# Optimization experiments

Measured on AMD Instinct MI355X. Metric: run time of the kernel, lower is better.

Reference implementation:

```python
import jax, jax.numpy as jnp
import numpy as np
import math

N_HEADS = 4
N_KV_GROUPS = 1
HEAD_DIM = 256
SLIDING_WINDOW = 512
ROPE_BASE = 1000000.0
EPS = 1e-6


def _rmsnorm(x, gamma):
    # normalize over last dim (head_dim), torch nn.RMSNorm semantics
    ms = jnp.mean(jnp.square(x), axis=-1, keepdims=True)
    return x * jax.lax.rsqrt(ms + EPS) * gamma


def _rope_tables(T, head_dim, dtype):
    inv_freq = 1.0 / (ROPE_BASE ** (jnp.arange(0, head_dim, 2, dtype=jnp.float32) / head_dim))
    t = jnp.arange(T, dtype=jnp.float32)
    freqs = jnp.outer(t, inv_freq)          # [T, head_dim/2]
    return jnp.cos(freqs).astype(dtype), jnp.sin(freqs).astype(dtype)


def _apply_rope(x, cos, sin):
    # x: [B, T, H, hd]; cos/sin: [T, hd/2] broadcast as [1, T, 1, hd/2]
    x0 = x[..., 0::2]
    x1 = x[..., 1::2]
    c = cos[None, :, None, :]
    s = sin[None, :, None, :]
    even = x0 * c - x1 * s
    odd = x0 * s + x1 * c
    return jnp.stack((even, odd), axis=-1).reshape(x.shape)


def setup_inputs() -> dict:
    key = jax.random.key(0)
    ks = jax.random.split(key, 5)
    B, T, C = 2, 4096, 1024
    scale = 0.02
    return {
        "x": jax.random.normal(ks[0], (B, T, C), dtype=jnp.float32),
        "Wq": jax.random.normal(ks[1], (C, C), dtype=jnp.float32) * scale,
        "Wk": jax.random.normal(ks[2], (N_KV_GROUPS * HEAD_DIM, C), dtype=jnp.float32) * scale,
        "Wv": jax.random.normal(ks[3], (N_KV_GROUPS * HEAD_DIM, C), dtype=jnp.float32) * scale,
        "Wo": jax.random.normal(ks[4], (C, C), dtype=jnp.float32) * scale,
        "q_gamma": jnp.ones((HEAD_DIM,), dtype=jnp.float32),
        "k_gamma": jnp.ones((HEAD_DIM,), dtype=jnp.float32),
    }


def reference(x, Wq, Wk, Wv, Wo, q_gamma, k_gamma):
    B, T, C = x.shape
    H, G, hd = N_HEADS, N_KV_GROUPS, HEAD_DIM
    rep = H // G

    q = (x @ Wq.T).reshape(B, T, H, hd)
    k = (x @ Wk.T).reshape(B, T, G, hd)
    v = (x @ Wv.T).reshape(B, T, G, hd)

    q = _rmsnorm(q, q_gamma)
    k = _rmsnorm(k, k_gamma)

    cos, sin = _rope_tables(T, hd, q.dtype)
    q = _apply_rope(q, cos, sin)
    k = _apply_rope(k, cos, sin)

    q = q.transpose(0, 2, 1, 3)                 # [B, H, T, hd]
    k = k.transpose(0, 2, 1, 3)                 # [B, G, T, hd]
    v = v.transpose(0, 2, 1, 3)
    k = jnp.repeat(k, rep, axis=1)              # [B, H, T, hd]
    v = jnp.repeat(v, rep, axis=1)

    scores = jnp.einsum("bhqd,bhkd->bhqk", q, k) / math.sqrt(hd)
    i = jnp.arange(T)[:, None]
    j = jnp.arange(T)[None, :]
    allowed = (j <= i) & (j >= i - SLIDING_WINDOW)   # causal sliding window
    scores = jnp.where(allowed, scores, -jnp.inf)
    attn = jax.nn.softmax(scores, axis=-1)
    out = jnp.einsum("bhqk,bhkd->bhqd", attn, v)     # [B, H, T, hd]
    out = out.transpose(0, 2, 1, 3).reshape(B, T, C)
    return out @ Wo.T
```

## Files before the change

### kernel.cpp

```cpp
#include <hip/hip_runtime.h>
#include <cstdint>
#include <cstddef>

#define T_SEQ 4096
#define NB    2
#define CDIM  1024
#define HD    256
#define NH    4

typedef __attribute__((ext_vector_type(8))) __bf16 bf16x8;
typedef __attribute__((ext_vector_type(4))) __bf16 bf16x4;
typedef __attribute__((ext_vector_type(4))) float  floatx4;

__device__ __forceinline__ floatx4 mfma16(bf16x8 a, bf16x8 b, floatx4 c) {
  return __builtin_amdgcn_mfma_f32_16x16x32_bf16(a, b, c, 0, 0, 0);
}

__device__ __forceinline__ void gl2lds16(const void* g, void* l) {
  __builtin_amdgcn_global_load_lds(
      (__attribute__((address_space(1))) void*)g,
      (__attribute__((address_space(3))) void*)l, 16, 0, 0);
}

__global__ __launch_bounds__(256) void cvt_all(const float* __restrict__ x,
                                               const float* __restrict__ wq,
                                               const float* __restrict__ wk,
                                               const float* __restrict__ wv,
                                               const float* __restrict__ wo,
                                               __bf16* __restrict__ xb,
                                               __bf16* __restrict__ wb,
                                               __bf16* __restrict__ wob) {
  int i = blockIdx.x * 256 + threadIdx.x;
  const float* src;
  __bf16* dst;
  int off;
  if (i < 2097152)      { src = x;  dst = xb;            off = i; }
  else if (i < 2359296) { src = wq; dst = wb;            off = i - 2097152; }
  else if (i < 2424832) { src = wk; dst = wb + 1048576;  off = i - 2359296; }
  else if (i < 2490368) { src = wv; dst = wb + 1310720;  off = i - 2424832; }
  else                  { src = wo; dst = wob;           off = i - 2490368; }
  float4 v = ((const float4*)src)[off];
  bf16x4 o;
  o[0] = (__bf16)v.x; o[1] = (__bf16)v.y; o[2] = (__bf16)v.z; o[3] = (__bf16)v.w;
  *(bf16x4*)&dst[(size_t)off * 4] = o;
}

template <typename OutT>
__global__ __launch_bounds__(256) void gemm_bt(const __bf16* __restrict__ A,
                                               const __bf16* __restrict__ B,
                                               OutT* __restrict__ C,
                                               int M, int N, int K) {
  __shared__ __bf16 As[128 * 64];
  __shared__ __bf16 Bs[128 * 64];
  const int tid  = threadIdx.x;
  const int lane = tid & 63;
  const int wave = tid >> 6;
  const int wm = wave >> 1, wn = wave & 1;
  const int lrow = lane & 15, quad = lane >> 4;
  const int bm = blockIdx.y, bn = blockIdx.x;

  const __bf16* gA = A + (size_t)(bm * 128) * K;
  const __bf16* gB = B + (size_t)(bn * 128) * K;
  const int arow = tid >> 3;
  const int acol = ((tid & 7) ^ ((tid >> 3) & 7)) * 8;
  const int l7 = lrow & 7;

  floatx4 acc[4][4] = {};

  for (int kt = 0; kt < K; kt += 64) {
#pragma unroll
    for (int i = 0; i < 4; ++i)
      gl2lds16(gA + (size_t)(i * 32 + arow) * K + kt + acol, &As[i * 2048 + tid * 8]);
#pragma unroll
    for (int i = 0; i < 4; ++i)
      gl2lds16(gB + (size_t)(i * 32 + arow) * K + kt + acol, &Bs[i * 2048 + tid * 8]);
    __syncthreads();
#pragma unroll
    for (int kk = 0; kk < 2; ++kk) {
      bf16x8 af[4], bfr[4];
#pragma unroll
      for (int mi = 0; mi < 4; ++mi)
        af[mi] = *(const bf16x8*)&As[(wm * 64 + mi * 16 + lrow) * 64 +
                                     ((kk * 4 + quad) ^ l7) * 8];
#pragma unroll
      for (int ni = 0; ni < 4; ++ni)
        bfr[ni] = *(const bf16x8*)&Bs[(wn * 64 + ni * 16 + lrow) * 64 +
                                      ((kk * 4 + quad) ^ l7) * 8];
#pragma unroll
      for (int mi = 0; mi < 4; ++mi)
#pragma unroll
        for (int ni = 0; ni < 4; ++ni)
          acc[mi][ni] = mfma16(af[mi], bfr[ni], acc[mi][ni]);
    }
    __syncthreads();
  }

  const int row0 = bm * 128 + wm * 64;
  const int col0 = bn * 128 + wn * 64;
#pragma unroll
  for (int mi = 0; mi < 4; ++mi)
#pragma unroll
    for (int ni = 0; ni < 4; ++ni)
#pragma unroll
      for (int r = 0; r < 4; ++r) {
        int row = row0 + mi * 16 + quad * 4 + r;
        int col = col0 + ni * 16 + lrow;
        C[(size_t)row * N + col] = (OutT)acc[mi][ni][r];
      }
}

__global__ __launch_bounds__(256) void rmsrope(const __bf16* __restrict__ qkv,
                                               const float* __restrict__ qg,
                                               const float* __restrict__ kg,
                                               __bf16* __restrict__ qr,
                                               __bf16* __restrict__ kr,
                                               __bf16* __restrict__ vt) {
  __shared__ __bf16 Ls[64 * 256];
  if (blockIdx.x >= 5120) {
    const int vb = blockIdx.x - 5120;
    const int b = vb >> 6, tt = vb & 63;
    const int tid = threadIdx.x;
    const __bf16* src = qkv + ((size_t)(b * 4096 + tt * 64)) * 1536 + 1280;
#pragma unroll
    for (int i = 0; i < 8; ++i)
      gl2lds16(src + (size_t)(i * 8 + (tid >> 5)) * 1536 + (tid & 31) * 8,
               &Ls[i * 2048 + tid * 8]);
    __syncthreads();
    __bf16 buf[64];
#pragma unroll
    for (int i = 0; i < 64; ++i) buf[i] = Ls[i * 256 + tid];
    __bf16* dst = vt + ((size_t)(b * 256 + tid)) * T_SEQ + tt * 64;
#pragma unroll
    for (int i = 0; i < 8; ++i)
      *(bf16x8*)&dst[i * 8] = *(const bf16x8*)&buf[i * 8];
    return;
  }

  const int inst = blockIdx.x * 4 + (threadIdx.x >> 6);
  const int lane = threadIdx.x & 63;
  const int rp = inst / 5, which = inst - rp * 5;
  const int row = rp * 2 + (lane >> 5);
  const int hl = lane & 31;
  const int b = row >> 12, t = row & 4095;

  const int srcoff = (which < 4) ? which * 256 : 1024;
  const __bf16* src = qkv + (size_t)row * 1536 + srcoff;
  bf16x8 xv = *(const bf16x8*)&src[hl * 8];

  float xf[8];
  float ss = 0.f;
#pragma unroll
  for (int j = 0; j < 8; ++j) { xf[j] = (float)xv[j]; ss += xf[j] * xf[j]; }
#pragma unroll
  for (int off = 16; off >= 1; off >>= 1) ss += __shfl_xor(ss, off);
  const float rms = rsqrtf(ss * (1.0f / 256.0f) + 1e-6f);

  const float* g = (which < 4) ? qg : kg;
  const float4 gv0 = *(const float4*)&g[hl * 8];
  const float4 gv1 = *(const float4*)&g[hl * 8 + 4];
  float y[8];
  y[0] = xf[0] * rms * gv0.x; y[1] = xf[1] * rms * gv0.y;
  y[2] = xf[2] * rms * gv0.z; y[3] = xf[3] * rms * gv0.w;
  y[4] = xf[4] * rms * gv1.x; y[5] = xf[5] * rms * gv1.y;
  y[6] = xf[6] * rms * gv1.z; y[7] = xf[7] * rms * gv1.w;

  const float c_log2 = -19.931568569324174f / 128.0f;
  bf16x8 ov;
#pragma unroll
  for (int j = 0; j < 4; ++j) {
    const int p = hl * 4 + j;
    const float a = (float)t * exp2f((float)p * c_log2);
    const float sn = __sinf(a), cs = __cosf(a);
    ov[2 * j]     = (__bf16)(y[2 * j] * cs - y[2 * j + 1] * sn);
    ov[2 * j + 1] = (__bf16)(y[2 * j] * sn + y[2 * j + 1] * cs);
  }

  __bf16* dst = (which < 4)
      ? qr + ((size_t)((b * NH + which) * T_SEQ) + t) * 256
      : kr + ((size_t)(b * T_SEQ) + t) * 256;
  *(bf16x8*)&dst[hl * 8] = ov;
}

__global__ __launch_bounds__(256, 2) void attn(const __bf16* __restrict__ qr,
                                               const __bf16* __restrict__ kr,
                                               const __bf16* __restrict__ vt,
                                               __bf16* __restrict__ ao) {
  __shared__ __bf16 Ks[2][32 * 256];
  __shared__ __bf16 Vs[2][256 * 32];
  __shared__ __bf16 Ps[2][64 * 32];

  const int bid = ((blockIdx.x & 7) << 6) | (blockIdx.x >> 3);
  const int qi = bid & 63, h = (bid >> 6) & 3, b = bid >> 8;
  const int tid = threadIdx.x, wave = tid >> 6, lane = tid & 63;
  const int wq = wave & 1, wk = wave >> 1;
  const int lrow = lane & 15, quad = lane >> 4;
  const int l7 = lrow & 7;

  const __bf16* Q = qr + (size_t)((b * NH + h) * T_SEQ) * 256;
  const __bf16* K = kr + (size_t)(b * T_SEQ) * 256;
  const __bf16* V = vt + (size_t)(b * 256) * T_SEQ;

  const int qbase = qi * 64;

  bf16x8 qf[2][8];
#pragma unroll
  for (int qt = 0; qt < 2; ++qt)
#pragma unroll
    for (int c = 0; c < 8; ++c)
      qf[qt][c] = *(const bf16x8*)&Q[(size_t)(qbase + wq * 32 + qt * 16 + lrow) * 256 +
                                     c * 32 + quad * 8];

  bf16x8 onesv;
#pragma unroll
  for (int j = 0; j < 8; ++j) onesv[j] = (__bf16)1.0f;

  floatx4 o[2][8] = {};
  floatx4 lm[2] = {};

  const int jt0 = (qi >= 8) ? 2 * qi - 16 : 0;
  const int jt1 = 2 * qi + 1;

  const int krow = tid >> 5;
  const int kcol = ((tid & 31) ^ (krow & 7)) * 8;
  const int vrow = tid >> 2;
  const int vcol = ((tid & 3) ^ ((vrow ^ (vrow >> 2)) & 3)) * 8;

#pragma unroll
  for (int i = 0; i < 4; ++i)
    gl2lds16(K + (size_t)(jt0 * 32 + i * 8 + krow) * 256 + kcol,
             &Ks[jt0 & 1][i * 2048 + tid * 8]);
#pragma unroll
  for (int i = 0; i < 4; ++i)
    gl2lds16(V + (size_t)(i * 64 + vrow) * T_SEQ + jt0 * 32 + vcol,
             &Vs[jt0 & 1][i * 2048 + tid * 8]);
#pragma unroll
  for (int i = 0; i < 4; ++i)
    gl2lds16(K + (size_t)((jt0 + 1) * 32 + i * 8 + krow) * 256 + kcol,
             &Ks[(jt0 + 1) & 1][i * 2048 + tid * 8]);

  for (int jt = jt0; jt <= jt1; ++jt) {
    if (jt < jt1) {
      asm volatile("s_waitcnt vmcnt(8)\n\ts_barrier" ::: "memory");
    } else {
      asm volatile("s_waitcnt vmcnt(4)\n\ts_barrier" ::: "memory");
    }

    const __bf16* Kb = Ks[jt & 1];

    floatx4 s[2] = {};
    __builtin_amdgcn_s_setprio(1);
#pragma unroll
    for (int c = 0; c < 8; ++c) {
      bf16x8 kf = *(const bf16x8*)&Kb[(wk * 16 + lrow) * 256 +
                                      ((c * 4 + quad) ^ l7) * 8];
      s[0] = mfma16(kf, qf[0][c], s[0]);
      s[1] = mfma16(kf, qf[1][c], s[1]);
    }
    __builtin_amdgcn_s_setprio(0);

    const bool full = (jt <= 2 * qi - 1) && (jt >= 2 * qi - 14);

    const float C1 = 0.09016844005556021f;
    const float C2 = 23.083120654223415f;
    __bf16* Pb = Ps[jt & 1];
#pragma unroll
    for (int qt = 0; qt < 2; ++qt) {
      bf16x4 pk;
#pragma unroll
      for (int r = 0; r < 4; ++r) {
        float v = s[qt][r];
        if (!full) {
          const int jk = jt * 32 + wk * 16 + quad * 4 + r;
          const int iq = qbase + wq * 32 + qt * 16 + lrow;
          v = ((jk <= iq) && (jk + 512 >= iq)) ? v : -1e30f;
        }
        pk[r] = (__bf16)exp2f(v * C1 - C2);
      }
      const int q = wq * 32 + qt * 16 + lrow;
      const int chunk = (wk * 2 + (quad >> 1)) ^ ((q ^ (q >> 2)) & 3);
      *(bf16x4*)((char*)Pb + q * 64 + chunk * 16 + (quad & 1) * 8) = pk;
    }

    if (jt < jt1) {
      asm volatile("s_waitcnt lgkmcnt(0) vmcnt(4)\n\ts_barrier" ::: "memory");
    } else {
      asm volatile("s_waitcnt lgkmcnt(0) vmcnt(0)\n\ts_barrier" ::: "memory");
    }

    if (jt + 1 <= jt1) {
#pragma unroll
      for (int i = 0; i < 4; ++i)
        gl2lds16(V + (size_t)(i * 64 + vrow) * T_SEQ + (jt + 1) * 32 + vcol,
                 &Vs[(jt + 1) & 1][i * 2048 + tid * 8]);
    }
    if (jt + 2 <= jt1) {
#pragma unroll
      for (int i = 0; i < 4; ++i)
        gl2lds16(K + (size_t)((jt + 2) * 32 + i * 8 + krow) * 256 + kcol,
                 &Ks[jt & 1][i * 2048 + tid * 8]);
    }

    bf16x8 pf[2];
#pragma unroll
    for (int qt = 0; qt < 2; ++qt) {
      const int q = wq * 32 + qt * 16 + lrow;
      pf[qt] = *(const bf16x8*)((char*)Pb + q * 64 +
                                (quad ^ ((q ^ (q >> 2)) & 3)) * 16);
    }

    __builtin_amdgcn_s_setprio(1);
    lm[0] = mfma16(pf[0], onesv, lm[0]);
    lm[1] = mfma16(pf[1], onesv, lm[1]);

    const __bf16* Vb = Vs[jt & 1];
#pragma unroll
    for (int n = 0; n < 8; ++n) {
      const int row = wk * 128 + n * 16 + lrow;
      bf16x8 vf = *(const bf16x8*)&Vb[row * 32 +
                                      ((quad ^ ((row ^ (row >> 2)) & 3)) * 8)];
      o[0][n] = mfma16(pf[0], vf, o[0][n]);
      o[1][n] = mfma16(pf[1], vf, o[1][n]);
    }
    __builtin_amdgcn_s_setprio(0);
  }

#pragma unroll
  for (int qt = 0; qt < 2; ++qt)
#pragma unroll
    for (int r = 0; r < 4; ++r) {
      const float rl = 1.0f / lm[qt][r];
      const int tg = qbase + wq * 32 + qt * 16 + quad * 4 + r;
#pragma unroll
      for (int n = 0; n < 8; ++n)
        ao[((size_t)(b * T_SEQ + tg)) * CDIM + h * 256 + wk * 128 + n * 16 + lrow] =
            (__bf16)(o[qt][n][r] * rl);
    }
}

extern "C" void kernel_launch(void* const* d_in, const int* in_sizes, int n_in,
                              void* d_out, int out_size, void* d_ws, size_t ws_size,
                              hipStream_t stream) {
  const float* x  = (const float*)d_in[0];
  const float* Wq = (const float*)d_in[1];
  const float* Wk = (const float*)d_in[2];
  const float* Wv = (const float*)d_in[3];
  const float* Wo = (const float*)d_in[4];
  const float* qg = (const float*)d_in[5];
  const float* kg = (const float*)d_in[6];
  float* out = (float*)d_out;

  const size_t M = (size_t)NB * T_SEQ;
  char* ws = (char*)d_ws;
  __bf16* xb  = (__bf16*)ws; ws += M * CDIM * 2;
  __bf16* wb  = (__bf16*)ws; ws += (size_t)1536 * CDIM * 2;
  __bf16* wob = (__bf16*)ws; ws += (size_t)CDIM * CDIM * 2;
  __bf16* qkv = (__bf16*)ws; ws += M * 1536 * 2;
  __bf16* qr  = (__bf16*)ws; ws += M * CDIM * 2;
  __bf16* kr  = (__bf16*)ws; ws += M * HD * 2;
  __bf16* vt  = (__bf16*)ws; ws += M * HD * 2;
  __bf16* ao  = (__bf16*)ws;

  cvt_all<<<10752, 256, 0, stream>>>(x, Wq, Wk, Wv, Wo, xb, wb, wob);

  gemm_bt<__bf16><<<dim3(12, 64), 256, 0, stream>>>(xb, wb, qkv, 8192, 1536, 1024);

  rmsrope<<<5248, 256, 0, stream>>>(qkv, qg, kg, qr, kr, vt);

  attn<<<NB * NH * (T_SEQ / 64), 256, 0, stream>>>(qr, kr, vt, ao);

  gemm_bt<float><<<dim3(8, 64), 256, 0, stream>>>(ao, wob, out, 8192, 1024, 1024);
}
```

Baseline: 209.6 us.

## Split attention block across eight waves with sixteen query rows each

Doubles attention workgroup size to 512 threads so each wave owns 16 query rows instead of 32, halving per-thread accumulators and Q fragments. Cooperative K/V tile loads are redistributed to two chunks per thread, and vmcnt waits are adjusted. This aims for more latency hiding via more waves, at the cost of each wave re-reading the full K/V fragments from LDS for half the MFMA work, doubling LDS read traffic per block.

```diff
diff --git a/kernel.cpp b/kernel.cpp
--- a/kernel.cpp
+++ b/kernel.cpp
@@ -181,7 +181,7 @@
   *(bf16x8*)&dst[hl * 8] = ov;
 }
 
-__global__ __launch_bounds__(256, 2) void attn(const __bf16* __restrict__ qr,
+__global__ __launch_bounds__(512, 4) void attn(const __bf16* __restrict__ qr,
                                                const __bf16* __restrict__ kr,
                                                const __bf16* __restrict__ vt,
                                                __bf16* __restrict__ ao) {
@@ -192,7 +192,8 @@
   const int bid = ((blockIdx.x & 7) << 6) | (blockIdx.x >> 3);
   const int qi = bid & 63, h = (bid >> 6) & 3, b = bid >> 8;
   const int tid = threadIdx.x, wave = tid >> 6, lane = tid & 63;
-  const int wq = wave & 1, wk = wave >> 1;
+  const int wq = wave & 3;
+  const int wk = wave >> 2;
   const int lrow = lane & 15, quad = lane >> 4;
   const int l7 = lrow & 7;
 
@@ -202,20 +203,18 @@
 
   const int qbase = qi * 64;
 
-  bf16x8 qf[2][8];
-#pragma unroll
-  for (int qt = 0; qt < 2; ++qt)
-#pragma unroll
-    for (int c = 0; c < 8; ++c)
-      qf[qt][c] = *(const bf16x8*)&Q[(size_t)(qbase + wq * 32 + qt * 16 + lrow) * 256 +
-                                     c * 32 + quad * 8];
+  bf16x8 qf[8];
+#pragma unroll
+  for (int c = 0; c < 8; ++c)
+    qf[c] = *(const bf16x8*)&Q[(size_t)(qbase + wq * 16 + lrow) * 256 +
+                               c * 32 + quad * 8];
 
   bf16x8 onesv;
 #pragma unroll
   for (int j = 0; j < 8; ++j) onesv[j] = (__bf16)1.0f;
 
-  floatx4 o[2][8] = {};
-  floatx4 lm[2] = {};
+  floatx4 o[8] = {};
+  floatx4 lm = {};
 
   const int jt0 = (qi >= 8) ? 2 * qi - 16 : 0;
   const int jt1 = 2 * qi + 1;
@@ -226,35 +225,34 @@
   const int vcol = ((tid & 3) ^ ((vrow ^ (vrow >> 2)) & 3)) * 8;
 
 #pragma unroll
-  for (int i = 0; i < 4; ++i)
-    gl2lds16(K + (size_t)(jt0 * 32 + i * 8 + krow) * 256 + kcol,
-             &Ks[jt0 & 1][i * 2048 + tid * 8]);
-#pragma unroll
-  for (int i = 0; i < 4; ++i)
-    gl2lds16(V + (size_t)(i * 64 + vrow) * T_SEQ + jt0 * 32 + vcol,
-             &Vs[jt0 & 1][i * 2048 + tid * 8]);
-#pragma unroll
-  for (int i = 0; i < 4; ++i)
-    gl2lds16(K + (size_t)((jt0 + 1) * 32 + i * 8 + krow) * 256 + kcol,
-             &Ks[(jt0 + 1) & 1][i * 2048 + tid * 8]);
+  for (int i = 0; i < 2; ++i)
+    gl2lds16(K + (size_t)(jt0 * 32 + i * 16 + krow) * 256 + kcol,
+             &Ks[jt0 & 1][i * 4096 + tid * 8]);
+#pragma unroll
+  for (int i = 0; i < 2; ++i)
+    gl2lds16(V + (size_t)(i * 128 + vrow) * T_SEQ + jt0 * 32 + vcol,
+             &Vs[jt0 & 1][i * 4096 + tid * 8]);
+#pragma unroll
+  for (int i = 0; i < 2; ++i)
+    gl2lds16(K + (size_t)((jt0 + 1) * 32 + i * 16 + krow) * 256 + kcol,
+             &Ks[(jt0 + 1) & 1][i * 4096 + tid * 8]);
 
   for (int jt = jt0; jt <= jt1; ++jt) {
     if (jt < jt1) {
-      asm volatile("s_waitcnt vmcnt(8)\n\ts_barrier" ::: "memory");
+      asm volatile("s_waitcnt vmcnt(4)\n\ts_barrier" ::: "memory");
     } else {
-      asm volatile("s_waitcnt vmcnt(4)\n\ts_barrier" ::: "memory");
+      asm volatile("s_waitcnt vmcnt(2)\n\ts_barrier" ::: "memory");
     }
 
     const __bf16* Kb = Ks[jt & 1];
 
-    floatx4 s[2] = {};
+    floatx4 s = {};
     __builtin_amdgcn_s_setprio(1);
 #pragma unroll
     for (int c = 0; c < 8; ++c) {
       bf16x8 kf = *(const bf16x8*)&Kb[(wk * 16 + lrow) * 256 +
                                       ((c * 4 + quad) ^ l7) * 8];
-      s[0] = mfma16(kf, qf[0][c], s[0]);
-      s[1] = mfma16(kf, qf[1][c], s[1]);
+      s = mfma16(kf, qf[c], s);
     }
     __builtin_amdgcn_s_setprio(0);
 
@@ -263,54 +261,51 @@
     const float C1 = 0.09016844005556021f;
     const float C2 = 23.083120654223415f;
     __bf16* Pb = Ps[jt & 1];
-#pragma unroll
-    for (int qt = 0; qt < 2; ++qt) {
+    {
       bf16x4 pk;
 #pragma unroll
       for (int r = 0; r < 4; ++r) {
-        float v = s[qt][r];
+        float v = s[r];
         if (!full) {
           const int jk = jt * 32 + wk * 16 + quad * 4 + r;
-          const int iq = qbase + wq * 32 + qt * 16 + lrow;
+          const int iq = qbase + wq * 16 + lrow;
           v = ((jk <= iq) && (jk + 512 >= iq)) ? v : -1e30f;
         }
         pk[r] = (__bf16)exp2f(v * C1 - C2);
       }
-      const int q = wq * 32 + qt * 16 + lrow;
+      const int q = wq * 16 + lrow;
       const int chunk = (wk * 2 + (quad >> 1)) ^ ((q ^ (q >> 2)) & 3);
       *(bf16x4*)((char*)Pb + q * 64 + chunk * 16 + (quad & 1) * 8) = pk;
     }
 
     if (jt < jt1) {
-      asm volatile("s_waitcnt lgkmcnt(0) vmcnt(4)\n\ts_barrier" ::: "memory");
+      asm volatile("s_waitcnt lgkmcnt(0) vmcnt(2)\n\ts_barrier" ::: "memory");
     } else {
       asm volatile("s_waitcnt lgkmcnt(0) vmcnt(0)\n\ts_barrier" ::: "memory");
     }
 
     if (jt + 1 <= jt1) {
 #pragma unroll
-      for (int i = 0; i < 4; ++i)
-        gl2lds16(V + (size_t)(i * 64 + vrow) * T_SEQ + (jt + 1) * 32 + vcol,
-                 &Vs[(jt + 1) & 1][i * 2048 + tid * 8]);
+      for (int i = 0; i < 2; ++i)
+        gl2lds16(V + (size_t)(i * 128 + vrow) * T_SEQ + (jt + 1) * 32 + vcol,
+                 &Vs[(jt + 1) & 1][i * 4096 + tid * 8]);
     }
     if (jt + 2 <= jt1) {
 #pragma unroll
-      for (int i = 0; i < 4; ++i)
-        gl2lds16(K + (size_t)((jt + 2) * 32 + i * 8 + krow) * 256 + kcol,
-                 &Ks[jt & 1][i * 2048 + tid * 8]);
-    }
-
-    bf16x8 pf[2];
-#pragma unroll
-    for (int qt = 0; qt < 2; ++qt) {
-      const int q = wq * 32 + qt * 16 + lrow;
-      pf[qt] = *(const bf16x8*)((char*)Pb + q * 64 +
-                                (quad ^ ((q ^ (q >> 2)) & 3)) * 16);
+      for (int i = 0; i < 2; ++i)
+        gl2lds16(K + (size_t)((jt + 2) * 32 + i * 16 + krow) * 256 + kcol,
+                 &Ks[jt & 1][i * 4096 + tid * 8]);
+    }
+
+    bf16x8 pf;
+    {
+      const int q = wq * 16 + lrow;
+      pf = *(const bf16x8*)((char*)Pb + q * 64 +
+                            (quad ^ ((q ^ (q >> 2)) & 3)) * 16);
     }
 
     __builtin_amdgcn_s_setprio(1);
-    lm[0] = mfma16(pf[0], onesv, lm[0]);
-    lm[1] = mfma16(pf[1], onesv, lm[1]);
+    lm = mfma16(pf, onesv, lm);
 
     const __bf16* Vb = Vs[jt & 1];
 #pragma unroll
@@ -318,23 +313,20 @@
       const int row = wk * 128 + n * 16 + lrow;
       bf16x8 vf = *(const bf16x8*)&Vb[row * 32 +
                                       ((quad ^ ((row ^ (row >> 2)) & 3)) * 8)];
-      o[0][n] = mfma16(pf[0], vf, o[0][n]);
-      o[1][n] = mfma16(pf[1], vf, o[1][n]);
+      o[n] = mfma16(pf, vf, o[n]);
     }
     __builtin_amdgcn_s_setprio(0);
   }
 
 #pragma unroll
-  for (int qt = 0; qt < 2; ++qt)
-#pragma unroll
-    for (int r = 0; r < 4; ++r) {
-      const float rl = 1.0f / lm[qt][r];
-      const int tg = qbase + wq * 32 + qt * 16 + quad * 4 + r;
-#pragma unroll
-      for (int n = 0; n < 8; ++n)
-        ao[((size_t)(b * T_SEQ + tg)) * CDIM + h * 256 + wk * 128 + n * 16 + lrow] =
-            (__bf16)(o[qt][n][r] * rl);
-    }
+  for (int r = 0; r < 4; ++r) {
+    const float rl = 1.0f / lm[r];
+    const int tg = qbase + wq * 16 + quad * 4 + r;
+#pragma unroll
+    for (int n = 0; n < 8; ++n)
+      ao[((size_t)(b * T_SEQ + tg)) * CDIM + h * 256 + wk * 128 + n * 16 + lrow] =
+          (__bf16)(o[n][r] * rl);
+  }
 }
 
 extern "C" void kernel_launch(void* const* d_in, const int* in_sizes, int n_in,
@@ -366,7 +358,7 @@
 
   rmsrope<<<5248, 256, 0, stream>>>(qkv, qg, kg, qr, kr, vt);
 
-  attn<<<NB * NH * (T_SEQ / 64), 256, 0, stream>>>(qr, kr, vt, ao);
+  attn<<<NB * NH * (T_SEQ / 64), 512, 0, stream>>>(qr, kr, vt, ao);
 
   gemm_bt<float><<<dim3(8, 64), 256, 0, stream>>>(ao, wob, out, 8192, 1024, 1024);
 }
```

After: 208.6 us. About the same (-0.5%).

## Warp-specialize attention into QK/softmax producer and PV consumer waves

Applied to the files above, without the earlier changes.

The attention block grows from 256 to 512 threads and splits its waves into two roles. Waves 0-3 load K tiles and compute QK^T plus the exp into the shared P buffer. Waves 4-7 load V tiles and accumulate P·V one tile behind, so that score/softmax work overlaps with the PV MFMAs through double-buffered LDS and one barrier per step. The risks are heavier register and LDS demand per block (launch bounds request 4 blocks of 512 threads) and load imbalance between the two roles.

```diff
diff --git a/kernel.cpp b/kernel.cpp
--- a/kernel.cpp
+++ b/kernel.cpp
@@ -181,7 +181,7 @@
   *(bf16x8*)&dst[hl * 8] = ov;
 }
 
-__global__ __launch_bounds__(256, 2) void attn(const __bf16* __restrict__ qr,
+__global__ __launch_bounds__(512, 4) void attn(const __bf16* __restrict__ qr,
                                                const __bf16* __restrict__ kr,
                                                const __bf16* __restrict__ vt,
                                                __bf16* __restrict__ ao) {
@@ -192,7 +192,6 @@
   const int bid = ((blockIdx.x & 7) << 6) | (blockIdx.x >> 3);
   const int qi = bid & 63, h = (bid >> 6) & 3, b = bid >> 8;
   const int tid = threadIdx.x, wave = tid >> 6, lane = tid & 63;
-  const int wq = wave & 1, wk = wave >> 1;
   const int lrow = lane & 15, quad = lane >> 4;
   const int l7 = lrow & 7;
 
@@ -201,140 +200,141 @@
   const __bf16* V = vt + (size_t)(b * 256) * T_SEQ;
 
   const int qbase = qi * 64;
-
-  bf16x8 qf[2][8];
-#pragma unroll
-  for (int qt = 0; qt < 2; ++qt)
-#pragma unroll
-    for (int c = 0; c < 8; ++c)
-      qf[qt][c] = *(const bf16x8*)&Q[(size_t)(qbase + wq * 32 + qt * 16 + lrow) * 256 +
-                                     c * 32 + quad * 8];
-
-  bf16x8 onesv;
-#pragma unroll
-  for (int j = 0; j < 8; ++j) onesv[j] = (__bf16)1.0f;
-
-  floatx4 o[2][8] = {};
-  floatx4 lm[2] = {};
-
   const int jt0 = (qi >= 8) ? 2 * qi - 16 : 0;
   const int jt1 = 2 * qi + 1;
-
-  const int krow = tid >> 5;
-  const int kcol = ((tid & 31) ^ (krow & 7)) * 8;
-  const int vrow = tid >> 2;
-  const int vcol = ((tid & 3) ^ ((vrow ^ (vrow >> 2)) & 3)) * 8;
-
-#pragma unroll
-  for (int i = 0; i < 4; ++i)
-    gl2lds16(K + (size_t)(jt0 * 32 + i * 8 + krow) * 256 + kcol,
-             &Ks[jt0 & 1][i * 2048 + tid * 8]);
-#pragma unroll
-  for (int i = 0; i < 4; ++i)
-    gl2lds16(V + (size_t)(i * 64 + vrow) * T_SEQ + jt0 * 32 + vcol,
-             &Vs[jt0 & 1][i * 2048 + tid * 8]);
-#pragma unroll
-  for (int i = 0; i < 4; ++i)
-    gl2lds16(K + (size_t)((jt0 + 1) * 32 + i * 8 + krow) * 256 + kcol,
-             &Ks[(jt0 + 1) & 1][i * 2048 + tid * 8]);
-
-  for (int jt = jt0; jt <= jt1; ++jt) {
-    if (jt < jt1) {
-      asm volatile("s_waitcnt vmcnt(8)\n\ts_barrier" ::: "memory");
-    } else {
-      asm volatile("s_waitcnt vmcnt(4)\n\ts_barrier" ::: "memory");
+  const int NT = jt1 - jt0 + 1;
+
+  if (wave < 4) {
+    const int kb = wave & 1, qh = wave >> 1;
+    const int t = tid;
+    const int krow = t >> 5;
+    const int kcol = ((t & 31) ^ krow) * 8;
+
+    bf16x8 qf[2][8];
+#pragma unroll
+    for (int qt = 0; qt < 2; ++qt)
+#pragma unroll
+      for (int c = 0; c < 8; ++c)
+        qf[qt][c] = *(const bf16x8*)&Q[(size_t)(qbase + qh * 32 + qt * 16 + lrow) * 256 +
+                                       c * 32 + quad * 8];
+
+#pragma unroll
+    for (int i = 0; i < 4; ++i)
+      gl2lds16(K + (size_t)(jt0 * 32 + i * 8 + krow) * 256 + kcol,
+               &Ks[jt0 & 1][i * 2048 + t * 8]);
+
+    for (int jt = jt0; jt <= jt1; ++jt) {
+      if (jt < jt1) {
+#pragma unroll
+        for (int i = 0; i < 4; ++i)
+          gl2lds16(K + (size_t)((jt + 1) * 32 + i * 8 + krow) * 256 + kcol,
+                   &Ks[(jt + 1) & 1][i * 2048 + t * 8]);
+        asm volatile("s_waitcnt vmcnt(4)" ::: "memory");
+      } else {
+        asm volatile("s_waitcnt vmcnt(0)" ::: "memory");
+      }
+
+      const __bf16* Kb = Ks[jt & 1];
+      floatx4 s[2] = {};
+      __builtin_amdgcn_s_setprio(1);
+#pragma unroll
+      for (int c = 0; c < 8; ++c) {
+        bf16x8 kf = *(const bf16x8*)&Kb[(kb * 16 + lrow) * 256 +
+                                        ((c * 4 + quad) ^ l7) * 8];
+        s[0] = mfma16(kf, qf[0][c], s[0]);
+        s[1] = mfma16(kf, qf[1][c], s[1]);
+      }
+      __builtin_amdgcn_s_setprio(0);
+
+      const bool full = (jt <= 2 * qi - 1) && (jt >= 2 * qi - 14);
+      const float C1 = 0.09016844005556021f;
+      const float C2 = 23.083120654223415f;
+      __bf16* Pb = Ps[jt & 1];
+#pragma unroll
+      for (int qt = 0; qt < 2; ++qt) {
+        bf16x4 pk;
+#pragma unroll
+        for (int r = 0; r < 4; ++r) {
+          float v = s[qt][r];
+          if (!full) {
+            const int jk = jt * 32 + kb * 16 + quad * 4 + r;
+            const int iq = qbase + qh * 32 + qt * 16 + lrow;
+            v = ((jk <= iq) && (jk + 512 >= iq)) ? v : -1e30f;
+          }
+          pk[r] = (__bf16)exp2f(v * C1 - C2);
+        }
+        const int q = qh * 32 + qt * 16 + lrow;
+        const int chunk = (kb * 2 + (quad >> 1)) ^ ((q ^ (q >> 2)) & 3);
+        *(bf16x4*)((char*)Pb + q * 64 + chunk * 16 + (quad & 1) * 8) = pk;
+      }
+      asm volatile("s_waitcnt lgkmcnt(0)\n\ts_barrier" ::: "memory");
     }
-
-    const __bf16* Kb = Ks[jt & 1];
-
-    floatx4 s[2] = {};
-    __builtin_amdgcn_s_setprio(1);
-#pragma unroll
-    for (int c = 0; c < 8; ++c) {
-      bf16x8 kf = *(const bf16x8*)&Kb[(wk * 16 + lrow) * 256 +
-                                      ((c * 4 + quad) ^ l7) * 8];
-      s[0] = mfma16(kf, qf[0][c], s[0]);
-      s[1] = mfma16(kf, qf[1][c], s[1]);
+  } else {
+    const int dw = wave - 4;
+    const int t = tid - 256;
+    const int vrow4 = t >> 2;
+    const int vcol = ((t & 3) ^ ((vrow4 ^ (vrow4 >> 2)) & 3)) * 8;
+
+    bf16x8 onesv;
+#pragma unroll
+    for (int j = 0; j < 8; ++j) onesv[j] = (__bf16)1.0f;
+
+    floatx4 o[4][4] = {};
+    floatx4 lm[4] = {};
+
+    for (int ii = 0; ii <= NT; ++ii) {
+      const int jt = jt0 + ii;
+      const int jp = jt - 1;
+      if (jt <= jt1) {
+#pragma unroll
+        for (int i = 0; i < 4; ++i)
+          gl2lds16(V + (size_t)(i * 64 + vrow4) * T_SEQ + jt * 32 + vcol,
+                   &Vs[jt & 1][i * 2048 + t * 8]);
+        asm volatile("s_waitcnt vmcnt(4)" ::: "memory");
+      } else {
+        asm volatile("s_waitcnt vmcnt(0)" ::: "memory");
+      }
+
+      if (ii >= 1) {
+        const __bf16* Pb = Ps[jp & 1];
+        const __bf16* Vb = Vs[jp & 1];
+        bf16x8 pf[4];
+#pragma unroll
+        for (int qt = 0; qt < 4; ++qt) {
+          const int q = qt * 16 + lrow;
+          pf[qt] = *(const bf16x8*)((char*)Pb + q * 64 +
+                                    (quad ^ ((q ^ (q >> 2)) & 3)) * 16);
+        }
+        __builtin_amdgcn_s_setprio(1);
+#pragma unroll
+        for (int qt = 0; qt < 4; ++qt) lm[qt] = mfma16(pf[qt], onesv, lm[qt]);
+#pragma unroll
+        for (int n = 0; n < 4; ++n) {
+          const int row = dw * 64 + n * 16 + lrow;
+          bf16x8 vf = *(const bf16x8*)&Vb[row * 32 +
+                                          ((quad ^ ((row ^ (row >> 2)) & 3)) * 8)];
+#pragma unroll
+          for (int qt = 0; qt < 4; ++qt)
+            o[qt][n] = mfma16(pf[qt], vf, o[qt][n]);
+        }
+        __builtin_amdgcn_s_setprio(0);
+      }
+      if (ii < NT)
+        asm volatile("s_waitcnt lgkmcnt(0)\n\ts_barrier" ::: "memory");
     }
-    __builtin_amdgcn_s_setprio(0);
-
-    const bool full = (jt <= 2 * qi - 1) && (jt >= 2 * qi - 14);
-
-    const float C1 = 0.09016844005556021f;
-    const float C2 = 23.083120654223415f;
-    __bf16* Pb = Ps[jt & 1];
-#pragma unroll
-    for (int qt = 0; qt < 2; ++qt) {
-      bf16x4 pk;
+
+#pragma unroll
+    for (int qt = 0; qt < 4; ++qt)
 #pragma unroll
       for (int r = 0; r < 4; ++r) {
-        float v = s[qt][r];
-        if (!full) {
-          const int jk = jt * 32 + wk * 16 + quad * 4 + r;
-          const int iq = qbase + wq * 32 + qt * 16 + lrow;
-          v = ((jk <= iq) && (jk + 512 >= iq)) ? v : -1e30f;
-        }
-        pk[r] = (__bf16)exp2f(v * C1 - C2);
-      }
-      const int q = wq * 32 + qt * 16 + lrow;
-      const int chunk = (wk * 2 + (quad >> 1)) ^ ((q ^ (q >> 2)) & 3);
-      *(bf16x4*)((char*)Pb + q * 64 + chunk * 16 + (quad & 1) * 8) = pk;
-    }
-
-    if (jt < jt1) {
-      asm volatile("s_waitcnt lgkmcnt(0) vmcnt(4)\n\ts_barrier" ::: "memory");
-    } else {
-      asm volatile("s_waitcnt lgkmcnt(0) vmcnt(0)\n\ts_barrier" ::: "memory");
-    }
-
-    if (jt + 1 <= jt1) {
-#pragma unroll
-      for (int i = 0; i < 4; ++i)
-        gl2lds16(V + (size_t)(i * 64 + vrow) * T_SEQ + (jt + 1) * 32 + vcol,
-                 &Vs[(jt + 1) & 1][i * 2048 + tid * 8]);
-    }
-    if (jt + 2 <= jt1) {
-#pragma unroll
-      for (int i = 0; i < 4; ++i)
-        gl2lds16(K + (size_t)((jt + 2) * 32 + i * 8 + krow) * 256 + kcol,
-                 &Ks[jt & 1][i * 2048 + tid * 8]);
-    }
-
-    bf16x8 pf[2];
-#pragma unroll
-    for (int qt = 0; qt < 2; ++qt) {
-      const int q = wq * 32 + qt * 16 + lrow;
-      pf[qt] = *(const bf16x8*)((char*)Pb + q * 64 +
-                                (quad ^ ((q ^ (q >> 2)) & 3)) * 16);
-    }
-
-    __builtin_amdgcn_s_setprio(1);
-    lm[0] = mfma16(pf[0], onesv, lm[0]);
-    lm[1] = mfma16(pf[1], onesv, lm[1]);
-
-    const __bf16* Vb = Vs[jt & 1];
-#pragma unroll
-    for (int n = 0; n < 8; ++n) {
-      const int row = wk * 128 + n * 16 + lrow;
-      bf16x8 vf = *(const bf16x8*)&Vb[row * 32 +
-                                      ((quad ^ ((row ^ (row >> 2)) & 3)) * 8)];
-      o[0][n] = mfma16(pf[0], vf, o[0][n]);
-      o[1][n] = mfma16(pf[1], vf, o[1][n]);
-    }
-    __builtin_amdgcn_s_setprio(0);
+        const float rl = 1.0f / lm[qt][r];
+        const int tg = qbase + qt * 16 + quad * 4 + r;
+#pragma unroll
+        for (int n = 0; n < 4; ++n)
+          ao[((size_t)(b * T_SEQ + tg)) * CDIM + h * 256 + dw * 64 + n * 16 + lrow] =
+              (__bf16)(o[qt][n][r] * rl);
+      }
   }
-
-#pragma unroll
-  for (int qt = 0; qt < 2; ++qt)
-#pragma unroll
-    for (int r = 0; r < 4; ++r) {
-      const float rl = 1.0f / lm[qt][r];
-      const int tg = qbase + wq * 32 + qt * 16 + quad * 4 + r;
-#pragma unroll
-      for (int n = 0; n < 8; ++n)
-        ao[((size_t)(b * T_SEQ + tg)) * CDIM + h * 256 + wk * 128 + n * 16 + lrow] =
-            (__bf16)(o[qt][n][r] * rl);
-    }
 }
 
 extern "C" void kernel_launch(void* const* d_in, const int* in_sizes, int n_in,
@@ -366,7 +366,7 @@
 
   rmsrope<<<5248, 256, 0, stream>>>(qkv, qg, kg, qr, kr, vt);
 
-  attn<<<NB * NH * (T_SEQ / 64), 256, 0, stream>>>(qr, kr, vt, ao);
+  attn<<<NB * NH * (T_SEQ / 64), 512, 0, stream>>>(qr, kr, vt, ao);
 
   gemm_bt<float><<<dim3(8, 64), 256, 0, stream>>>(ao, wob, out, 8192, 1024, 1024);
 }
```

Result: faster. 205.3 us (-2.0%).
